# Optimization experiments

Hardware: AMD Instinct MI355X
Metric: run time of the kernel (lower is better)

Reference implementation:

```python
import jax, jax.numpy as jnp
import numpy as np

IN_FEATURES = 4096
OUT_FEATURES = 4096
N_TOKENS = 8192


def setup_inputs() -> dict:
    key = jax.random.key(0)
    kx, kw = jax.random.split(key)
    x = jax.random.normal(kx, (N_TOKENS, IN_FEATURES), dtype=jnp.float32)
    # weight = randn(out, in) * 0.1, bias = zeros(out), per BinaryLinear.__init__
    weight = jax.random.normal(kw, (OUT_FEATURES, IN_FEATURES), dtype=jnp.float32) * 0.1
    bias = jnp.zeros((OUT_FEATURES,), dtype=jnp.float32)
    return {"x": x, "weight": weight, "bias": bias}


def reference(x, weight, bias):
    # sign-binarize weights (torch .sign(): -1/0/+1, matched by jnp.sign),
    # then dense linear: x @ sign(W)^T + b
    bin_w = jnp.sign(weight)
    return jnp.einsum('ni,oi->no', x, bin_w) + bias
```

## Files before the change

kernel.cpp:

```cpp
#include <hip/hip_runtime.h>
#include <stdint.h>

typedef __attribute__((ext_vector_type(4))) int   i32x4;

#define M_TOK 8192
#define N_OUT 4096
#define K_IN  4096

#define BM 128
#define BN 128
#define BK 64

#define GLDS16(gp, lp)                                                         \
  __builtin_amdgcn_global_load_lds(                                            \
      (const __attribute__((address_space(1))) void*)(gp),                     \
      (__attribute__((address_space(3))) void*)(lp), 16, 0, 0)

__global__ void __launch_bounds__(256) quant_x_i8(const float* __restrict__ x,
                                                  char* __restrict__ xq,
                                                  float* __restrict__ scales) {
  const int row = blockIdx.x;
  const int t   = threadIdx.x;
  const float* rp = x + (size_t)row * K_IN + t * 16;

  float v[16];
#pragma unroll
  for (int p = 0; p < 4; p++) {
    float4 f = ((const float4*)rp)[p];
    v[p * 4 + 0] = f.x; v[p * 4 + 1] = f.y; v[p * 4 + 2] = f.z; v[p * 4 + 3] = f.w;
  }
  float amax = 0.f;
#pragma unroll
  for (int i = 0; i < 16; i++) amax = fmaxf(amax, fabsf(v[i]));

#pragma unroll
  for (int off = 32; off > 0; off >>= 1)
    amax = fmaxf(amax, __shfl_xor(amax, off));

  __shared__ float wmax[4];
  if ((t & 63) == 0) wmax[t >> 6] = amax;
  __syncthreads();
  amax = fmaxf(fmaxf(wmax[0], wmax[1]), fmaxf(wmax[2], wmax[3]));
  amax = fmaxf(amax, 1e-30f);

  const float inv = 127.f / amax;
  if (t == 0) scales[row] = amax / 127.f;

  uint32_t o[4];
#pragma unroll
  for (int p = 0; p < 4; p++) {
    uint32_t b0 = (uint32_t)(__float2int_rn(v[p * 4 + 0] * inv) & 0xFF);
    uint32_t b1 = (uint32_t)(__float2int_rn(v[p * 4 + 1] * inv) & 0xFF);
    uint32_t b2 = (uint32_t)(__float2int_rn(v[p * 4 + 2] * inv) & 0xFF);
    uint32_t b3 = (uint32_t)(__float2int_rn(v[p * 4 + 3] * inv) & 0xFF);
    o[p] = b0 | (b1 << 8) | (b2 << 16) | (b3 << 24);
  }
  uint4 pk; pk.x = o[0]; pk.y = o[1]; pk.z = o[2]; pk.w = o[3];
  ((uint4*)(xq + (size_t)row * K_IN + t * 16))[0] = pk;
}

__global__ void __launch_bounds__(256) quant_w_sign(const float* __restrict__ w,
                                                    char* __restrict__ wq, int n16) {
  int i = blockIdx.x * 256 + threadIdx.x;
  if (i >= n16) return;
  const float4* p = (const float4*)w + (size_t)i * 4;
  uint32_t o[4];
#pragma unroll
  for (int q = 0; q < 4; q++) {
    float4 f = p[q];
    int s0 = (f.x > 0.f) - (f.x < 0.f);
    int s1 = (f.y > 0.f) - (f.y < 0.f);
    int s2 = (f.z > 0.f) - (f.z < 0.f);
    int s3 = (f.w > 0.f) - (f.w < 0.f);
    o[q] = (uint32_t)(s0 & 0xFF) | ((uint32_t)(s1 & 0xFF) << 8) |
           ((uint32_t)(s2 & 0xFF) << 16) | ((uint32_t)(s3 & 0xFF) << 24);
  }
  uint4 pk; pk.x = o[0]; pk.y = o[1]; pk.z = o[2]; pk.w = o[3];
  ((uint4*)wq)[i] = pk;
}

__global__ void __launch_bounds__(256) gemm_bin_i8(
    const char* __restrict__ A, const char* __restrict__ B,
    const float* __restrict__ scales, const float* __restrict__ bias,
    float* __restrict__ C) {
  __shared__ char sA[BM * BK];
  __shared__ char sB[BN * BK];

  const int tid  = threadIdx.x;
  const int lane = tid & 63;
  const int wv   = tid >> 6;
  const int wr   = wv >> 1;
  const int wc   = wv & 1;

  const int m0 = blockIdx.y * BM;
  const int n0 = blockIdx.x * BN;

  const int ldRow = lane >> 2;
  const int ldK   = (lane & 3) * 16;
  const char* gA = A + (size_t)(m0 + wv * 32 + ldRow) * K_IN + ldK;
  const char* gB = B + (size_t)(n0 + wv * 32 + ldRow) * K_IN + ldK;
  char* lA0 = &sA[(wv * 32 +  0) * BK];
  char* lA1 = &sA[(wv * 32 + 16) * BK];
  char* lB0 = &sB[(wv * 32 +  0) * BK];
  char* lB1 = &sB[(wv * 32 + 16) * BK];

  i32x4 acc[4][4];
#pragma unroll
  for (int i = 0; i < 4; i++)
#pragma unroll
    for (int j = 0; j < 4; j++) acc[i][j] = (i32x4){0, 0, 0, 0};

  const int fragK = (lane >> 4) * 16;
  const int fragR = lane & 15;

  for (int k0 = 0; k0 < K_IN; k0 += BK) {
    GLDS16(gA + k0,             lA0);
    GLDS16(gA + k0 + 16 * K_IN, lA1);
    GLDS16(gB + k0,             lB0);
    GLDS16(gB + k0 + 16 * K_IN, lB1);
    __syncthreads();

    i32x4 aF[4], bF[4];
#pragma unroll
    for (int mi = 0; mi < 4; mi++)
      aF[mi] = *(const i32x4*)&sA[(wr * 64 + mi * 16 + fragR) * BK + fragK];
#pragma unroll
    for (int ni = 0; ni < 4; ni++)
      bF[ni] = *(const i32x4*)&sB[(wc * 64 + ni * 16 + fragR) * BK + fragK];

#pragma unroll
    for (int mi = 0; mi < 4; mi++)
#pragma unroll
      for (int ni = 0; ni < 4; ni++)
        acc[mi][ni] = __builtin_amdgcn_mfma_i32_16x16x64_i8(
            aF[mi], bF[ni], acc[mi][ni], 0, 0, 0);

    __syncthreads();
  }

#pragma unroll
  for (int ni = 0; ni < 4; ni++) {
    const int col = n0 + wc * 64 + ni * 16 + (lane & 15);
    const float bv = bias[col];
#pragma unroll
    for (int mi = 0; mi < 4; mi++) {
      const int row0 = m0 + wr * 64 + mi * 16 + (lane >> 4) * 4;
      float* cp = C + (size_t)row0 * N_OUT + col;
#pragma unroll
      for (int r = 0; r < 4; r++)
        cp[(size_t)r * N_OUT] = (float)acc[mi][ni][r] * scales[row0 + r] + bv;
    }
  }
}

__global__ void fallback_gemm(const float* __restrict__ x, const float* __restrict__ w,
                              const float* __restrict__ bias, float* __restrict__ out) {
  int idx = blockIdx.x * blockDim.x + threadIdx.x;
  if (idx >= M_TOK * N_OUT) return;
  int row = idx / N_OUT, col = idx % N_OUT;
  const float* xp = x + (size_t)row * K_IN;
  const float* wp = w + (size_t)col * K_IN;
  float s = 0.f;
  for (int k = 0; k < K_IN; k++) {
    float wv = wp[k];
    float sg = wv > 0.f ? 1.f : (wv < 0.f ? -1.f : 0.f);
    s += xp[k] * sg;
  }
  out[idx] = s + bias[col];
}

extern "C" void kernel_launch(void* const* d_in, const int* in_sizes, int n_in,
                              void* d_out, int out_size, void* d_ws, size_t ws_size,
                              hipStream_t stream) {
  const float* x    = (const float*)d_in[0];
  const float* w    = (const float*)d_in[1];
  const float* bias = (const float*)d_in[2];
  float* out = (float*)d_out;

  const size_t xq_bytes = (size_t)M_TOK * K_IN;
  const size_t wq_bytes = (size_t)N_OUT * K_IN;
  const size_t sc_bytes = (size_t)M_TOK * sizeof(float);

  if (ws_size < xq_bytes + wq_bytes + sc_bytes) {
    int total = M_TOK * N_OUT;
    fallback_gemm<<<(total + 255) / 256, 256, 0, stream>>>(x, w, bias, out);
    return;
  }

  char*  xq = (char*)d_ws;
  char*  wq = (char*)d_ws + xq_bytes;
  float* sc = (float*)((char*)d_ws + xq_bytes + wq_bytes);

  quant_x_i8<<<M_TOK, 256, 0, stream>>>(x, xq, sc);
  {
    int n16 = N_OUT * K_IN / 16;
    quant_w_sign<<<(n16 + 255) / 256, 256, 0, stream>>>(w, wq, n16);
  }
  dim3 grid(N_OUT / BN, M_TOK / BM);
  gemm_bin_i8<<<grid, 256, 0, stream>>>(xq, wq, sc, bias, out);
}
```

Before: 435.4 us.

## Switch GEMM to 32x32x32 int8 MFMA with BK=128 and XOR-swizzled LDS

The int8 GEMM moves from 16x16x64 MFMA tiles to 32x32x32 MFMA tiles and doubles the K step to 128. LDS is laid out with an XOR swizzle on 16-byte chunks to avoid bank conflicts on fragment reads. The epilogue is adjusted to the 32x32 accumulator layout. Both quantization kernels now use coalesced per-thread strided float4 loads and 4-byte stores instead of each thread handling a contiguous 64-byte run. The aim is to cut barrier and loop overhead per K, reduce LDS bank conflicts and improve load coalescing, at the risk of different register pressure and occupancy.

```diff
diff --git a/kernel.cpp b/kernel.cpp
--- a/kernel.cpp
+++ b/kernel.cpp
@@ -1,7 +1,8 @@
 #include <hip/hip_runtime.h>
 #include <stdint.h>
 
-typedef __attribute__((ext_vector_type(4))) int   i32x4;
+typedef __attribute__((ext_vector_type(4)))  int i32x4;
+typedef __attribute__((ext_vector_type(16))) int i32x16;
 
 #define M_TOK 8192
 #define N_OUT 4096
@@ -9,7 +10,7 @@
 
 #define BM 128
 #define BN 128
-#define BK 64
+#define BK 128
 
 #define GLDS16(gp, lp)                                                         \
   __builtin_amdgcn_global_load_lds(                                            \
@@ -21,17 +22,17 @@
                                                   float* __restrict__ scales) {
   const int row = blockIdx.x;
   const int t   = threadIdx.x;
-  const float* rp = x + (size_t)row * K_IN + t * 16;
-
-  float v[16];
-#pragma unroll
-  for (int p = 0; p < 4; p++) {
-    float4 f = ((const float4*)rp)[p];
-    v[p * 4 + 0] = f.x; v[p * 4 + 1] = f.y; v[p * 4 + 2] = f.z; v[p * 4 + 3] = f.w;
-  }
+  const float4* rp = (const float4*)(x + (size_t)row * K_IN);
+
+  float4 v[4];
+#pragma unroll
+  for (int p = 0; p < 4; p++) v[p] = rp[p * 256 + t];
+
   float amax = 0.f;
 #pragma unroll
-  for (int i = 0; i < 16; i++) amax = fmaxf(amax, fabsf(v[i]));
+  for (int p = 0; p < 4; p++)
+    amax = fmaxf(amax, fmaxf(fmaxf(fabsf(v[p].x), fabsf(v[p].y)),
+                             fmaxf(fabsf(v[p].z), fabsf(v[p].w))));
 
 #pragma unroll
   for (int off = 32; off > 0; off >>= 1)
@@ -46,37 +47,33 @@
   const float inv = 127.f / amax;
   if (t == 0) scales[row] = amax / 127.f;
 
-  uint32_t o[4];
+  uint32_t* op = (uint32_t*)(xq + (size_t)row * K_IN);
 #pragma unroll
   for (int p = 0; p < 4; p++) {
-    uint32_t b0 = (uint32_t)(__float2int_rn(v[p * 4 + 0] * inv) & 0xFF);
-    uint32_t b1 = (uint32_t)(__float2int_rn(v[p * 4 + 1] * inv) & 0xFF);
-    uint32_t b2 = (uint32_t)(__float2int_rn(v[p * 4 + 2] * inv) & 0xFF);
-    uint32_t b3 = (uint32_t)(__float2int_rn(v[p * 4 + 3] * inv) & 0xFF);
-    o[p] = b0 | (b1 << 8) | (b2 << 16) | (b3 << 24);
-  }
-  uint4 pk; pk.x = o[0]; pk.y = o[1]; pk.z = o[2]; pk.w = o[3];
-  ((uint4*)(xq + (size_t)row * K_IN + t * 16))[0] = pk;
+    uint32_t b0 = (uint32_t)(__float2int_rn(v[p].x * inv) & 0xFF);
+    uint32_t b1 = (uint32_t)(__float2int_rn(v[p].y * inv) & 0xFF);
+    uint32_t b2 = (uint32_t)(__float2int_rn(v[p].z * inv) & 0xFF);
+    uint32_t b3 = (uint32_t)(__float2int_rn(v[p].w * inv) & 0xFF);
+    op[p * 256 + t] = b0 | (b1 << 8) | (b2 << 16) | (b3 << 24);
+  }
 }
 
 __global__ void __launch_bounds__(256) quant_w_sign(const float* __restrict__ w,
-                                                    char* __restrict__ wq, int n16) {
-  int i = blockIdx.x * 256 + threadIdx.x;
-  if (i >= n16) return;
-  const float4* p = (const float4*)w + (size_t)i * 4;
-  uint32_t o[4];
+                                                    char* __restrict__ wq) {
+  const int t = threadIdx.x;
+  const size_t base = (size_t)blockIdx.x * 1024;
+  const float4* p = (const float4*)w + base;
+  uint32_t* op = (uint32_t*)wq + base;
 #pragma unroll
   for (int q = 0; q < 4; q++) {
-    float4 f = p[q];
+    float4 f = p[q * 256 + t];
     int s0 = (f.x > 0.f) - (f.x < 0.f);
     int s1 = (f.y > 0.f) - (f.y < 0.f);
     int s2 = (f.z > 0.f) - (f.z < 0.f);
     int s3 = (f.w > 0.f) - (f.w < 0.f);
-    o[q] = (uint32_t)(s0 & 0xFF) | ((uint32_t)(s1 & 0xFF) << 8) |
-           ((uint32_t)(s2 & 0xFF) << 16) | ((uint32_t)(s3 & 0xFF) << 24);
-  }
-  uint4 pk; pk.x = o[0]; pk.y = o[1]; pk.z = o[2]; pk.w = o[3];
-  ((uint4*)wq)[i] = pk;
+    op[q * 256 + t] = (uint32_t)(s0 & 0xFF) | ((uint32_t)(s1 & 0xFF) << 8) |
+                      ((uint32_t)(s2 & 0xFF) << 16) | ((uint32_t)(s3 & 0xFF) << 24);
+  }
 }
 
 __global__ void __launch_bounds__(256) gemm_bin_i8(
@@ -95,60 +92,65 @@
   const int m0 = blockIdx.y * BM;
   const int n0 = blockIdx.x * BN;
 
-  const int ldRow = lane >> 2;
-  const int ldK   = (lane & 3) * 16;
-  const char* gA = A + (size_t)(m0 + wv * 32 + ldRow) * K_IN + ldK;
-  const char* gB = B + (size_t)(n0 + wv * 32 + ldRow) * K_IN + ldK;
-  char* lA0 = &sA[(wv * 32 +  0) * BK];
-  char* lA1 = &sA[(wv * 32 + 16) * BK];
-  char* lB0 = &sB[(wv * 32 +  0) * BK];
-  char* lB1 = &sB[(wv * 32 + 16) * BK];
-
-  i32x4 acc[4][4];
-#pragma unroll
-  for (int i = 0; i < 4; i++)
-#pragma unroll
-    for (int j = 0; j < 4; j++) acc[i][j] = (i32x4){0, 0, 0, 0};
-
-  const int fragK = (lane >> 4) * 16;
-  const int fragR = lane & 15;
+  const int srow   = lane >> 3;
+  const int schunk = (lane & 7) ^ srow;
+  const char* gA = A + (size_t)(m0 + wv * 32 + srow) * K_IN + schunk * 16;
+  const char* gB = B + (size_t)(n0 + wv * 32 + srow) * K_IN + schunk * 16;
+  char* lA = &sA[(wv * 32) * BK];
+  char* lB = &sB[(wv * 32) * BK];
+
+  i32x16 acc[2][2];
+#pragma unroll
+  for (int i = 0; i < 2; i++)
+#pragma unroll
+    for (int j = 0; j < 2; j++)
+#pragma unroll
+      for (int r = 0; r < 16; r++) acc[i][j][r] = 0;
+
+  const int fr  = lane & 31;
+  const int k16 = lane >> 5;
+  const int x7  = lane & 7;
+  const char* rA = &sA[(wr * 64 + fr) * BK];
+  const char* rB = &sB[(wc * 64 + fr) * BK];
 
   for (int k0 = 0; k0 < K_IN; k0 += BK) {
-    GLDS16(gA + k0,             lA0);
-    GLDS16(gA + k0 + 16 * K_IN, lA1);
-    GLDS16(gB + k0,             lB0);
-    GLDS16(gB + k0 + 16 * K_IN, lB1);
+#pragma unroll
+    for (int g = 0; g < 4; g++) {
+      GLDS16(gA + k0 + (size_t)(g * 8) * K_IN, lA + g * 8 * BK);
+      GLDS16(gB + k0 + (size_t)(g * 8) * K_IN, lB + g * 8 * BK);
+    }
     __syncthreads();
 
-    i32x4 aF[4], bF[4];
-#pragma unroll
-    for (int mi = 0; mi < 4; mi++)
-      aF[mi] = *(const i32x4*)&sA[(wr * 64 + mi * 16 + fragR) * BK + fragK];
-#pragma unroll
-    for (int ni = 0; ni < 4; ni++)
-      bF[ni] = *(const i32x4*)&sB[(wc * 64 + ni * 16 + fragR) * BK + fragK];
-
-#pragma unroll
-    for (int mi = 0; mi < 4; mi++)
-#pragma unroll
-      for (int ni = 0; ni < 4; ni++)
-        acc[mi][ni] = __builtin_amdgcn_mfma_i32_16x16x64_i8(
-            aF[mi], bF[ni], acc[mi][ni], 0, 0, 0);
-
+#pragma unroll
+    for (int ks = 0; ks < 4; ks++) {
+      const int soff = ((ks * 2 + k16) ^ x7) << 4;
+      i32x4 aF[2], bF[2];
+      aF[0] = *(const i32x4*)(rA + soff);
+      aF[1] = *(const i32x4*)(rA + 32 * BK + soff);
+      bF[0] = *(const i32x4*)(rB + soff);
+      bF[1] = *(const i32x4*)(rB + 32 * BK + soff);
+#pragma unroll
+      for (int mi = 0; mi < 2; mi++)
+#pragma unroll
+        for (int ni = 0; ni < 2; ni++)
+          acc[mi][ni] = __builtin_amdgcn_mfma_i32_32x32x32_i8(
+              aF[mi], bF[ni], acc[mi][ni], 0, 0, 0);
+    }
     __syncthreads();
   }
 
 #pragma unroll
-  for (int ni = 0; ni < 4; ni++) {
-    const int col = n0 + wc * 64 + ni * 16 + (lane & 15);
+  for (int ni = 0; ni < 2; ni++) {
+    const int col = n0 + wc * 64 + ni * 32 + (lane & 31);
     const float bv = bias[col];
 #pragma unroll
-    for (int mi = 0; mi < 4; mi++) {
-      const int row0 = m0 + wr * 64 + mi * 16 + (lane >> 4) * 4;
-      float* cp = C + (size_t)row0 * N_OUT + col;
-#pragma unroll
-      for (int r = 0; r < 4; r++)
-        cp[(size_t)r * N_OUT] = (float)acc[mi][ni][r] * scales[row0 + r] + bv;
+    for (int mi = 0; mi < 2; mi++) {
+      const int rbase = m0 + wr * 64 + mi * 32 + (lane >> 5) * 4;
+#pragma unroll
+      for (int r = 0; r < 16; r++) {
+        const int row = rbase + (r & 3) + 8 * (r >> 2);
+        C[(size_t)row * N_OUT + col] = (float)acc[mi][ni][r] * scales[row] + bv;
+      }
     }
   }
 }
@@ -192,10 +194,8 @@
   float* sc = (float*)((char*)d_ws + xq_bytes + wq_bytes);
 
   quant_x_i8<<<M_TOK, 256, 0, stream>>>(x, xq, sc);
-  {
-    int n16 = N_OUT * K_IN / 16;
-    quant_w_sign<<<(n16 + 255) / 256, 256, 0, stream>>>(w, wq, n16);
-  }
+  quant_w_sign<<<(N_OUT * K_IN / 4) / 1024, 256, 0, stream>>>(w, wq);
+
   dim3 grid(N_OUT / BN, M_TOK / BM);
   gemm_bin_i8<<<grid, 256, 0, stream>>>(xq, wq, sc, bias, out);
 }
```

New measurement: 405.1 us. 1.07x faster.
